# Performance work log

Hardware: AMD Instinct MI355X
Metric: run time of the kernel (lower is better)

## Reference

```python
import jax, jax.numpy as jnp
import numpy as np

N = 4096        # number of nodes
C = 512         # in_features
L_LAT = 64      # L_latent
EPS = 0.25      # epsilon


def setup_inputs() -> dict:
    key = jax.random.key(0)
    ks = jax.random.split(key, 8)
    def lin(k, fan_in, shape):
        return (jax.random.normal(k, shape, jnp.float32) / np.float32(np.sqrt(fan_in)))
    x = jax.random.normal(ks[0], (N, C), jnp.float32)
    adj = jax.random.uniform(ks[1], (N, N), jnp.float32)  # dense nonneg kernel
    W_proj = lin(ks[2], C, (C, L_LAT)); b_proj = jnp.zeros((L_LAT,), jnp.float32)
    W_pi1 = lin(ks[3], L_LAT, (L_LAT, C)); b_pi1 = jnp.zeros((C,), jnp.float32)
    W_pi2 = lin(ks[4], C, (C, 1)); b_pi2 = jnp.zeros((1,), jnp.float32)
    W_f = lin(ks[5], C, (C, C)); b_f = jnp.zeros((C,), jnp.float32)
    dt = jnp.array([0.1], jnp.float32)
    return {"x": x, "adj": adj, "W_proj": W_proj, "b_proj": b_proj,
            "W_pi1": W_pi1, "b_pi1": b_pi1, "W_pi2": W_pi2, "b_pi2": b_pi2,
            "W_f": W_f, "b_f": b_f, "dt": dt}


def reference(x, adj, W_proj, b_proj, W_pi1, b_pi1, W_pi2, b_pi2, W_f, b_f, dt):
    # proj_list: x -> latent [n, L]
    z = x @ W_proj + b_proj
    # pi_list: Linear -> ReLU -> Linear -> Sigmoid, squeeze to [n]
    pi = jax.nn.sigmoid(jax.nn.relu(z @ W_pi1 + b_pi1) @ W_pi2 + b_pi2)[:, 0]
    # q_epsilon_tilde: row sums of the kernel
    q = adj.sum(axis=1)                       # [n]
    # K_tilde = K_epsilon @ diag(pi/q)  == column scaling
    K_tilde = adj * (pi / q)[None, :]         # [n, n]
    # D_tilde diagonal; torch.inverse of a diagonal == elementwise reciprocal
    d = K_tilde.sum(axis=1) + 1e-5            # [n]
    # target = relu(f(x)) with f = Linear(C, C)
    target = jax.nn.relu(x @ W_f + b_f)       # [n, C]
    # L @ target = (1/eps) * diag(1/d) @ K_tilde @ target - target
    Lt = (K_tilde @ target) / (EPS * d)[:, None] - target
    return target + dt[0] * Lt
```

## Files before the change

### kernel.cpp

```cpp
#include <hip/hip_runtime.h>
#include <hip/hip_bf16.h>

#define N_NODES 4096
#define C_DIM   512
#define L_DIM   64
#define SPLITS  8
#define KCHUNK  (N_NODES / SPLITS)

typedef unsigned short u16;
using bf16x8 = __attribute__((ext_vector_type(8))) __bf16;
using u16x8  = __attribute__((ext_vector_type(8))) unsigned short;
using f32x4  = __attribute__((ext_vector_type(4))) float;

__device__ __forceinline__ float b2f(u16 u) {
    union { unsigned int i; float f; } v; v.i = ((unsigned int)u) << 16; return v.f;
}
__device__ __forceinline__ u16 f2b(float f) {
    unsigned int u = __float_as_uint(f);
    u += 0x7fff + ((u >> 16) & 1);
    return (u16)(u >> 16);
}

__device__ __forceinline__ void gload16(const u16* g, u16* l) {
    __builtin_amdgcn_global_load_lds((const __attribute__((address_space(1))) void*)g,
                                     (__attribute__((address_space(3))) void*)l,
                                     16, 0, 0);
}

__device__ __forceinline__ int detect_mode_inl(const u16* __restrict__ adj) {
    int m = 0;
#pragma unroll
    for (int i = 0; i < 64; ++i) m |= (adj[i] >= 0x8000) ? 1 : 0;
    return m;
}

#define OFF_DT    64
#define OFF_BIAS  1024
#define OFF_WP    4096
#define OFF_BP    135168
#define OFF_WP1   135424
#define OFF_BP1   266496
#define OFF_WP2   268544
#define OFF_BP2   270592
#define OFF_Q     271360
#define OFF_S     287744
#define OFF_DV    304128
#define OFF_T     1048576
#define OFF_TST   9437184
#define OFF_WFT   13631488
#define OFF_XB    14155776
#define OFF_ADJB  18350080

__device__ __forceinline__ float ldin(const void* p, int i, int mode) {
    if (mode) return ((const float*)p)[i];
    return b2f(((const u16*)p)[i]);
}

__global__ __launch_bounds__(256) void k1_prep(const void* __restrict__ adj, const void* __restrict__ x,
        const void* Wp, const void* bp, const void* Wp1, const void* bp1,
        const void* Wp2, const void* bp2, const void* Wf, const void* bfc, const void* dt,
        float* __restrict__ Wp_f, float* __restrict__ bp_f, float* __restrict__ Wp1_f,
        float* __restrict__ bp1_f, float* __restrict__ Wp2_f, float* __restrict__ bp2_f,
        float* __restrict__ bias_f, float* __restrict__ dt_f,
        u16* __restrict__ adjb, float* __restrict__ q, u16* __restrict__ xb,
        u16* __restrict__ WfT) {
    __shared__ float tile[32][33];
    int bid = blockIdx.x, tid = threadIdx.x;
    int mode = detect_mode_inl((const u16*)adj);
    if (bid < 263) {
        int idx = bid * 256 + tid;
        if (idx < 32768)        Wp_f[idx]          = ldin(Wp,  idx, mode);
        else if (idx < 32832)   bp_f[idx - 32768]  = ldin(bp,  idx - 32768, mode);
        else if (idx < 65600)   Wp1_f[idx - 32832] = ldin(Wp1, idx - 32832, mode);
        else if (idx < 66112)   bp1_f[idx - 65600] = ldin(bp1, idx - 65600, mode);
        else if (idx < 66624)   Wp2_f[idx - 66112] = ldin(Wp2, idx - 66112, mode);
        else if (idx == 66624)  bp2_f[0]           = ldin(bp2, 0, mode);
        else if (idx < 67137)   bias_f[idx - 66625] = ldin(bfc, idx - 66625, mode);
        else if (idx == 67137)  dt_f[0]            = ldin(dt, 0, mode);
    } else if (bid < 2311) {
        if (mode == 0) return;
        int idx = (bid - 263) * 256 + tid;
        float4 v = ((const float4*)x)[idx];
        ushort4 o; o.x = f2b(v.x); o.y = f2b(v.y); o.z = f2b(v.z); o.w = f2b(v.w);
        ((ushort4*)xb)[idx] = o;
    } else if (bid < 3335) {
        int wave = tid >> 6, lane = tid & 63;
        int row = (bid - 2311) * 4 + wave;
        float acc = 0.f;
        if (mode) {
            const float4* rp = (const float4*)((const float*)adj + (size_t)row * N_NODES);
            ushort4* wp = (ushort4*)(adjb + (size_t)row * N_NODES);
#pragma unroll
            for (int it = 0; it < 16; ++it) {
                float4 v = rp[it * 64 + lane];
                acc += v.x + v.y + v.z + v.w;
                ushort4 o; o.x = f2b(v.x); o.y = f2b(v.y); o.z = f2b(v.z); o.w = f2b(v.w);
                wp[it * 64 + lane] = o;
            }
        } else {
            const u16x8* rp = (const u16x8*)((const u16*)adj + (size_t)row * N_NODES);
#pragma unroll
            for (int it = 0; it < 8; ++it) {
                u16x8 v = rp[it * 64 + lane];
#pragma unroll
                for (int e = 0; e < 8; ++e) acc += b2f(v[e]);
            }
        }
#pragma unroll
        for (int off = 32; off > 0; off >>= 1) acc += __shfl_down(acc, off);
        if (lane == 0) q[row] = acc;
    } else {
        int g = bid - 3335;
        int tx = tid & 31, ty = tid >> 5;
        int x0 = (g & 15) * 32, y0 = (g >> 4) * 32;
        if (mode) {
            const float* src = (const float*)Wf;
#pragma unroll
            for (int r = ty; r < 32; r += 8) tile[r][tx] = src[(size_t)(y0 + r) * C_DIM + x0 + tx];
        } else {
            const u16* src = (const u16*)Wf;
#pragma unroll
            for (int r = ty; r < 32; r += 8) tile[r][tx] = b2f(src[(size_t)(y0 + r) * C_DIM + x0 + tx]);
        }
        __syncthreads();
#pragma unroll
        for (int r = ty; r < 32; r += 8)
            WfT[(size_t)(x0 + r) * C_DIM + y0 + tx] = f2b(tile[tx][r]);
    }
}

__global__ __launch_bounds__(256) void k2_pi_gemm1(const void* __restrict__ xraw,
        const u16* __restrict__ adjdet, const u16* __restrict__ xb, const u16* __restrict__ WfT,
        const float* __restrict__ Wp_f,  const float* __restrict__ bp_f,
        const float* __restrict__ Wp1_f, const float* __restrict__ bp1_f,
        const float* __restrict__ Wp2_f, const float* __restrict__ bp2_f,
        const float* __restrict__ bias_f, const float* __restrict__ dt_f,
        const float* __restrict__ q, float* __restrict__ s, float* __restrict__ T,
        void* __restrict__ out, float* __restrict__ Pacc) {
    __shared__ __align__(16) char smem[18560];
    int bid = blockIdx.x, tid = threadIdx.x;
    int mode = detect_mode_inl(adjdet);
    if (bid < 512) {
        float (*sx)[C_DIM] = (float(*)[C_DIM])smem;
        float (*sz)[L_DIM] = (float(*)[L_DIM])(smem + 16384);
        float (*red)[8]    = (float(*)[8])(smem + 18432);
        int i0 = bid * 8;
        if (mode) {
            const float4* xp = (const float4*)((const float*)xraw + (size_t)i0 * C_DIM);
            float4* sxf = (float4*)&sx[0][0];
#pragma unroll
            for (int r = 0; r < 4; ++r) sxf[tid + 256 * r] = xp[tid + 256 * r];
        } else {
            const u16x8* xp = (const u16x8*)((const u16*)xraw + (size_t)i0 * C_DIM);
#pragma unroll
            for (int r = 0; r < 2; ++r) {
                u16x8 v = xp[tid + 256 * r];
                float* dstf = &sx[0][0] + (size_t)(tid + 256 * r) * 8;
#pragma unroll
                for (int e = 0; e < 8; ++e) dstf[e] = b2f(v[e]);
            }
        }
        __syncthreads();
        int j = tid & 63, n0 = tid >> 6;
        float a0 = 0.f, a1 = 0.f;
#pragma unroll 4
        for (int k = 0; k < C_DIM; ++k) {
            float w = Wp_f[k * L_DIM + j];
            a0 += sx[n0][k] * w;
            a1 += sx[n0 + 4][k] * w;
        }
        sz[n0][j] = a0 + bp_f[j];
        sz[n0 + 4][j] = a1 + bp_f[j];
        __syncthreads();
        int m0 = tid, m1 = tid + 256;
        float b0 = bp1_f[m0], b1 = bp1_f[m1];
        float h0[8], h1[8];
#pragma unroll
        for (int n = 0; n < 8; ++n) { h0[n] = b0; h1[n] = b1; }
#pragma unroll 8
        for (int jj = 0; jj < L_DIM; ++jj) {
            float w0 = Wp1_f[jj * C_DIM + m0];
            float w1 = Wp1_f[jj * C_DIM + m1];
#pragma unroll
            for (int n = 0; n < 8; ++n) {
                float z = sz[n][jj];
                h0[n] += z * w0;
                h1[n] += z * w1;
            }
        }
        float w2a = Wp2_f[m0], w2b = Wp2_f[m1];
        float p[8];
#pragma unroll
        for (int n = 0; n < 8; ++n)
            p[n] = fmaxf(h0[n], 0.f) * w2a + fmaxf(h1[n], 0.f) * w2b;
#pragma unroll
        for (int off = 32; off > 0; off >>= 1)
#pragma unroll
            for (int n = 0; n < 8; ++n) p[n] += __shfl_down(p[n], off);
        int lane = tid & 63, wave = tid >> 6;
        if (lane == 0) {
#pragma unroll
            for (int n = 0; n < 8; ++n) red[wave][n] = p[n];
        }
        __syncthreads();
        if (tid < 8) {
            float tot = red[0][tid] + red[1][tid] + red[2][tid] + red[3][tid] + bp2_f[0];
            float pi = 1.f / (1.f + expf(-tot));
            s[i0 + tid] = pi / q[i0 + tid];
        }
    } else {
        u16* lA = (u16*)smem;
        u16* lB = (u16*)(smem + 4096);
        const u16* A = mode ? xb : (const u16*)xraw;
        float* tgt = mode ? (float*)out : Pacc;
        int g = bid - 512;
        int lane = tid & 63, wave = tid >> 6;
        int bm = (g & 63) * 64, bn = (g >> 6) * 64;
        int quad = lane >> 4, l15 = lane & 15;
        int wm = wave * 16;
        const u16* Ap = A + (size_t)(bm + (tid >> 2)) * C_DIM + (tid & 3) * 8;
        const u16* Bp = WfT + (size_t)(bn + (tid >> 2)) * C_DIM + (tid & 3) * 8;
        u16* la = lA + tid * 8;
        u16* lb = lB + tid * 8;
        f32x4 acc[4];
#pragma unroll
        for (int nt = 0; nt < 4; ++nt) acc[nt] = (f32x4){0.f, 0.f, 0.f, 0.f};
        for (int k0 = 0; k0 < C_DIM; k0 += 32) {
            gload16(Ap + k0, la);
            gload16(Bp + k0, lb);
            __syncthreads();
            bf16x8 af = *(const bf16x8*)&lA[(wm + l15) * 32 + quad * 8];
            bf16x8 bfv[4];
#pragma unroll
            for (int nt = 0; nt < 4; ++nt) bfv[nt] = *(const bf16x8*)&lB[(nt * 16 + l15) * 32 + quad * 8];
#pragma unroll
            for (int nt = 0; nt < 4; ++nt)
                acc[nt] = __builtin_amdgcn_mfma_f32_16x16x32_bf16(af, bfv[nt], acc[nt], 0, 0, 0);
            __syncthreads();
        }
        float c0 = 1.f - dt_f[0];
#pragma unroll
        for (int nt = 0; nt < 4; ++nt) {
            int col = bn + nt * 16 + l15;
            float bv = bias_f[col];
#pragma unroll
            for (int r = 0; r < 4; ++r) {
                int row = bm + wm + quad * 4 + r;
                float t = fmaxf(acc[nt][r] + bv, 0.f);
                T[(size_t)row * C_DIM + col] = t;
                tgt[(size_t)row * C_DIM + col] = c0 * t;
            }
        }
    }
}

__global__ __launch_bounds__(256) void k3_mid(const void* __restrict__ adjraw,
        const u16* __restrict__ adjb, const float* __restrict__ s,
        const float* __restrict__ T,
        float* __restrict__ dv, u16* __restrict__ TsT) {
    __shared__ float tile[32][33];
    int bid = blockIdx.x, tid = threadIdx.x;
    int mode = detect_mode_inl((const u16*)adjraw);
    if (bid < 1024) {
        const u16* A = mode ? adjb : (const u16*)adjraw;
        int wave = tid >> 6, lane = tid & 63;
        int row = bid * 4 + wave;
        const u16x8* rp = (const u16x8*)(A + (size_t)row * N_NODES);
        float acc = 0.f;
#pragma unroll
        for (int it = 0; it < 8; ++it) {
            int chunk = it * 64 + lane;
            u16x8 v = rp[chunk];
            const float4* sp = (const float4*)(s + chunk * 8);
            float4 s0 = sp[0], s1 = sp[1];
            acc += b2f(v[0]) * s0.x + b2f(v[1]) * s0.y + b2f(v[2]) * s0.z + b2f(v[3]) * s0.w;
            acc += b2f(v[4]) * s1.x + b2f(v[5]) * s1.y + b2f(v[6]) * s1.z + b2f(v[7]) * s1.w;
        }
#pragma unroll
        for (int off = 32; off > 0; off >>= 1) acc += __shfl_down(acc, off);
        if (lane == 0) dv[row] = acc + 1e-5f;
    } else {
        int g = bid - 1024;
        int tx = tid & 31, ty = tid >> 5;
        int x0 = (g & 15) * 32, y0 = (g >> 4) * 32;
#pragma unroll
        for (int r = ty; r < 32; r += 8) tile[r][tx] = T[(size_t)(y0 + r) * C_DIM + x0 + tx];
        __syncthreads();
        float sv = s[y0 + tx];
#pragma unroll
        for (int r = ty; r < 32; r += 8)
            TsT[(size_t)(x0 + r) * N_NODES + y0 + tx] = f2b(tile[tx][r] * sv);
    }
}

__global__ __launch_bounds__(256) void k4_gemm2(const void* __restrict__ adjraw,
        const u16* __restrict__ adjb, const u16* __restrict__ TsT,
        const float* __restrict__ dv, const float* __restrict__ dt_f,
        void* __restrict__ out, float* __restrict__ Pacc) {
    __shared__ __align__(16) u16 lA[128 * 32];
    __shared__ __align__(16) u16 lB[128 * 32];
    int mode = detect_mode_inl((const u16*)adjraw);
    const u16* A = mode ? adjb : (const u16*)adjraw;
    float* tgt = mode ? (float*)out : Pacc;
    int tid = threadIdx.x;
    int lane = tid & 63, wave = tid >> 6;
    int bm = blockIdx.x * 128, bn = blockIdx.y * 128;
    int kbase = blockIdx.z * KCHUNK;
    int wm = (wave & 1) * 64, wn = (wave >> 1) * 64;
    int quad = lane >> 4, l15 = lane & 15;

    const u16* Ab0 = A + (size_t)(bm + (tid >> 2)) * N_NODES + kbase + (tid & 3) * 8;
    const u16* Ab1 = A + (size_t)(bm + 64 + (tid >> 2)) * N_NODES + kbase + (tid & 3) * 8;
    const u16* Bb0 = TsT + (size_t)(bn + (tid >> 2)) * N_NODES + kbase + (tid & 3) * 8;
    const u16* Bb1 = TsT + (size_t)(bn + 64 + (tid >> 2)) * N_NODES + kbase + (tid & 3) * 8;
    u16* la0 = lA + tid * 8;  u16* la1 = lA + 2048 + tid * 8;
    u16* lb0 = lB + tid * 8;  u16* lb1 = lB + 2048 + tid * 8;

    f32x4 acc[4][4];
#pragma unroll
    for (int a = 0; a < 4; ++a)
#pragma unroll
        for (int b = 0; b < 4; ++b) acc[a][b] = (f32x4){0.f, 0.f, 0.f, 0.f};

    for (int k0 = 0; k0 < KCHUNK; k0 += 32) {
        gload16(Ab0 + k0, la0);
        gload16(Ab1 + k0, la1);
        gload16(Bb0 + k0, lb0);
        gload16(Bb1 + k0, lb1);
        __syncthreads();
        bf16x8 af[4], bfv[4];
#pragma unroll
        for (int mt = 0; mt < 4; ++mt) af[mt] = *(const bf16x8*)&lA[(wm + mt * 16 + l15) * 32 + quad * 8];
#pragma unroll
        for (int nt = 0; nt < 4; ++nt) bfv[nt] = *(const bf16x8*)&lB[(wn + nt * 16 + l15) * 32 + quad * 8];
#pragma unroll
        for (int mt = 0; mt < 4; ++mt)
#pragma unroll
            for (int nt = 0; nt < 4; ++nt)
                acc[mt][nt] = __builtin_amdgcn_mfma_f32_16x16x32_bf16(af[mt], bfv[nt], acc[mt][nt], 0, 0, 0);
        __syncthreads();
    }

    float c1 = dt_f[0] * 4.f;
#pragma unroll
    for (int mt = 0; mt < 4; ++mt) {
        float inv[4];
#pragma unroll
        for (int r = 0; r < 4; ++r) inv[r] = c1 / dv[bm + wm + mt * 16 + quad * 4 + r];
#pragma unroll
        for (int nt = 0; nt < 4; ++nt) {
            int col = bn + wn + nt * 16 + l15;
#pragma unroll
            for (int r = 0; r < 4; ++r) {
                int row = bm + wm + mt * 16 + quad * 4 + r;
                atomicAdd(&tgt[(size_t)row * C_DIM + col], acc[mt][nt][r] * inv[r]);
            }
        }
    }
}

__global__ __launch_bounds__(256) void k5_fin(const void* __restrict__ adjraw,
                                              const float* __restrict__ Pacc,
                                              u16* __restrict__ out) {
    if (detect_mode_inl((const u16*)adjraw)) return;
    int idx = blockIdx.x * 256 + threadIdx.x;
    float4 v = ((const float4*)Pacc)[idx];
    ushort4 o; o.x = f2b(v.x); o.y = f2b(v.y); o.z = f2b(v.z); o.w = f2b(v.w);
    ((ushort4*)out)[idx] = o;
}

extern "C" void kernel_launch(void* const* d_in, const int* in_sizes, int n_in,
                              void* d_out, int out_size, void* d_ws, size_t ws_size,
                              hipStream_t stream) {
    const void* x   = d_in[0];
    const void* adj = d_in[1];
    const void* Wp  = d_in[2];
    const void* bp  = d_in[3];
    const void* Wp1 = d_in[4];
    const void* bp1 = d_in[5];
    const void* Wp2 = d_in[6];
    const void* bp2 = d_in[7];
    const void* Wf  = d_in[8];
    const void* bfc = d_in[9];
    const void* dtp = d_in[10];
    const u16* adjdet = (const u16*)adj;

    char* ws = (char*)d_ws;
    float* dt_f   = (float*)(ws + OFF_DT);
    float* bias_f = (float*)(ws + OFF_BIAS);
    float* Wp_f   = (float*)(ws + OFF_WP);
    float* bp_f   = (float*)(ws + OFF_BP);
    float* Wp1_f  = (float*)(ws + OFF_WP1);
    float* bp1_f  = (float*)(ws + OFF_BP1);
    float* Wp2_f  = (float*)(ws + OFF_WP2);
    float* bp2_f  = (float*)(ws + OFF_BP2);
    float* q      = (float*)(ws + OFF_Q);
    float* s      = (float*)(ws + OFF_S);
    float* dv     = (float*)(ws + OFF_DV);
    float* T      = (float*)(ws + OFF_T);
    u16*   TsT    = (u16*)(ws + OFF_TST);
    u16*   WfT    = (u16*)(ws + OFF_WFT);
    u16*   xb     = (u16*)(ws + OFF_XB);
    u16*   adjb   = (u16*)(ws + OFF_ADJB);
    float* Pacc   = (float*)(ws + OFF_ADJB);

    k1_prep<<<3591, 256, 0, stream>>>(adj, x, Wp, bp, Wp1, bp1, Wp2, bp2, Wf, bfc, dtp,
                                      Wp_f, bp_f, Wp1_f, bp1_f, Wp2_f, bp2_f, bias_f, dt_f,
                                      adjb, q, xb, WfT);
    k2_pi_gemm1<<<1024, 256, 0, stream>>>(x, adjdet, xb, WfT,
                                          Wp_f, bp_f, Wp1_f, bp1_f, Wp2_f, bp2_f, bias_f, dt_f,
                                          q, s, T, d_out, Pacc);
    k3_mid<<<3072, 256, 0, stream>>>(adj, adjb, s, T, dv, TsT);
    k4_gemm2<<<dim3(32, 4, SPLITS), 256, 0, stream>>>(adj, adjb, TsT, dv, dt_f, d_out, Pacc);
    k5_fin<<<2048, 256, 0, stream>>>(adj, Pacc, (u16*)d_out);
}
```

Before: 253.5 us.

## Deepen GEMM2 K-step to 64, halve split-K, reuse bf16 x in projection

The main aggregation GEMM now stages two 32-wide K slices per iteration, which halves the number of barriers per K chunk. Split-K drops from 8 to 4, so each block covers a longer K range and issues fewer atomic adds to the output, at the cost of fewer blocks in flight. The projection kernel also reads the already-converted bf16 copy of x instead of fp32 x, which halves that load traffic. LDS use per GEMM block doubles, which may lower occupancy.

```diff
diff --git a/kernel.cpp b/kernel.cpp
--- a/kernel.cpp
+++ b/kernel.cpp
@@ -4,7 +4,7 @@
 #define N_NODES 4096
 #define C_DIM   512
 #define L_DIM   64
-#define SPLITS  8
+#define SPLITS  4
 #define KCHUNK  (N_NODES / SPLITS)
 
 typedef unsigned short u16;
@@ -145,20 +145,14 @@
         float (*sz)[L_DIM] = (float(*)[L_DIM])(smem + 16384);
         float (*red)[8]    = (float(*)[8])(smem + 18432);
         int i0 = bid * 8;
-        if (mode) {
-            const float4* xp = (const float4*)((const float*)xraw + (size_t)i0 * C_DIM);
-            float4* sxf = (float4*)&sx[0][0];
-#pragma unroll
-            for (int r = 0; r < 4; ++r) sxf[tid + 256 * r] = xp[tid + 256 * r];
-        } else {
-            const u16x8* xp = (const u16x8*)((const u16*)xraw + (size_t)i0 * C_DIM);
-#pragma unroll
-            for (int r = 0; r < 2; ++r) {
-                u16x8 v = xp[tid + 256 * r];
-                float* dstf = &sx[0][0] + (size_t)(tid + 256 * r) * 8;
-#pragma unroll
-                for (int e = 0; e < 8; ++e) dstf[e] = b2f(v[e]);
-            }
+        const u16* xsrc = mode ? xb : (const u16*)xraw;
+        const u16x8* xp = (const u16x8*)(xsrc + (size_t)i0 * C_DIM);
+#pragma unroll
+        for (int r = 0; r < 2; ++r) {
+            u16x8 v = xp[tid + 256 * r];
+            float* dstf = &sx[0][0] + (size_t)(tid + 256 * r) * 8;
+#pragma unroll
+            for (int e = 0; e < 8; ++e) dstf[e] = b2f(v[e]);
         }
         __syncthreads();
         int j = tid & 63, n0 = tid >> 6;
@@ -297,8 +291,8 @@
         const u16* __restrict__ adjb, const u16* __restrict__ TsT,
         const float* __restrict__ dv, const float* __restrict__ dt_f,
         void* __restrict__ out, float* __restrict__ Pacc) {
-    __shared__ __align__(16) u16 lA[128 * 32];
-    __shared__ __align__(16) u16 lB[128 * 32];
+    __shared__ __align__(16) u16 lA[8192];
+    __shared__ __align__(16) u16 lB[8192];
     int mode = detect_mode_inl((const u16*)adjraw);
     const u16* A = mode ? adjb : (const u16*)adjraw;
     float* tgt = mode ? (float*)out : Pacc;
@@ -313,8 +307,10 @@
     const u16* Ab1 = A + (size_t)(bm + 64 + (tid >> 2)) * N_NODES + kbase + (tid & 3) * 8;
     const u16* Bb0 = TsT + (size_t)(bn + (tid >> 2)) * N_NODES + kbase + (tid & 3) * 8;
     const u16* Bb1 = TsT + (size_t)(bn + 64 + (tid >> 2)) * N_NODES + kbase + (tid & 3) * 8;
-    u16* la0 = lA + tid * 8;  u16* la1 = lA + 2048 + tid * 8;
-    u16* lb0 = lB + tid * 8;  u16* lb1 = lB + 2048 + tid * 8;
+    u16* la00 = lA + tid * 8;        u16* la01 = lA + 2048 + tid * 8;
+    u16* la10 = lA + 4096 + tid * 8; u16* la11 = lA + 6144 + tid * 8;
+    u16* lb00 = lB + tid * 8;        u16* lb01 = lB + 2048 + tid * 8;
+    u16* lb10 = lB + 4096 + tid * 8; u16* lb11 = lB + 6144 + tid * 8;
 
     f32x4 acc[4][4];
 #pragma unroll
@@ -322,22 +318,31 @@
 #pragma unroll
         for (int b = 0; b < 4; ++b) acc[a][b] = (f32x4){0.f, 0.f, 0.f, 0.f};
 
-    for (int k0 = 0; k0 < KCHUNK; k0 += 32) {
-        gload16(Ab0 + k0, la0);
-        gload16(Ab1 + k0, la1);
-        gload16(Bb0 + k0, lb0);
-        gload16(Bb1 + k0, lb1);
-        __syncthreads();
-        bf16x8 af[4], bfv[4];
-#pragma unroll
-        for (int mt = 0; mt < 4; ++mt) af[mt] = *(const bf16x8*)&lA[(wm + mt * 16 + l15) * 32 + quad * 8];
-#pragma unroll
-        for (int nt = 0; nt < 4; ++nt) bfv[nt] = *(const bf16x8*)&lB[(wn + nt * 16 + l15) * 32 + quad * 8];
-#pragma unroll
-        for (int mt = 0; mt < 4; ++mt)
-#pragma unroll
-            for (int nt = 0; nt < 4; ++nt)
-                acc[mt][nt] = __builtin_amdgcn_mfma_f32_16x16x32_bf16(af[mt], bfv[nt], acc[mt][nt], 0, 0, 0);
+    for (int k0 = 0; k0 < KCHUNK; k0 += 64) {
+        gload16(Ab0 + k0, la00);
+        gload16(Ab1 + k0, la01);
+        gload16(Ab0 + k0 + 32, la10);
+        gload16(Ab1 + k0 + 32, la11);
+        gload16(Bb0 + k0, lb00);
+        gload16(Bb1 + k0, lb01);
+        gload16(Bb0 + k0 + 32, lb10);
+        gload16(Bb1 + k0 + 32, lb11);
+        __syncthreads();
+#pragma unroll
+        for (int kk = 0; kk < 2; ++kk) {
+            const u16* baseA = lA + kk * 4096;
+            const u16* baseB = lB + kk * 4096;
+            bf16x8 af[4], bfv[4];
+#pragma unroll
+            for (int mt = 0; mt < 4; ++mt) af[mt] = *(const bf16x8*)&baseA[(wm + mt * 16 + l15) * 32 + quad * 8];
+#pragma unroll
+            for (int nt = 0; nt < 4; ++nt) bfv[nt] = *(const bf16x8*)&baseB[(wn + nt * 16 + l15) * 32 + quad * 8];
+#pragma unroll
+            for (int mt = 0; mt < 4; ++mt)
+#pragma unroll
+                for (int nt = 0; nt < 4; ++nt)
+                    acc[mt][nt] = __builtin_amdgcn_mfma_f32_16x16x32_bf16(af[mt], bfv[nt], acc[mt][nt], 0, 0, 0);
+        }
         __syncthreads();
     }
 
```

New measurement: 227.5 us. 10.2% less time.
